# Kernel optimization log

Measured on AMD Instinct MI355X. Metric: run time of the kernel, lower is better.

The kernel has to match this reference:

```python
import jax, jax.numpy as jnp
import numpy as np

N_NODES = 50000
N_EDGES = 800000
D_FEAT = 128
D_HID = 500


def setup_inputs() -> dict:
    key = jax.random.key(0)
    k1, k2, k3, k4 = jax.random.split(key, 4)
    x = jax.random.normal(k1, (N_NODES, D_FEAT), dtype=jnp.float32)
    edge_index = jax.random.randint(k2, (2, N_EDGES), 0, N_NODES, dtype=jnp.int64)
    # Glorot-ish init for weights, zeros for bias (PyG GCNConv default)
    W1 = jax.random.normal(k3, (D_FEAT, D_HID), dtype=jnp.float32) / np.sqrt(D_FEAT)
    b1 = jnp.zeros((D_HID,), dtype=jnp.float32)
    W2 = jax.random.normal(k4, (D_HID, 1), dtype=jnp.float32) / np.sqrt(D_HID)
    b2 = jnp.zeros((1,), dtype=jnp.float32)
    return {"x": x, "edge_index": edge_index, "W1": W1, "b1": b1, "W2": W2, "b2": b2}


def gcn_conv(x, W, b, src, dst, n_nodes):
    """PyG GCNConv: linear transform, add self-loops, symmetric norm, scatter-add, bias."""
    h = x @ W  # [N, out]
    loops = jnp.arange(n_nodes, dtype=src.dtype)
    s = jnp.concatenate([src, loops])  # [E+N]
    d = jnp.concatenate([dst, loops])
    deg = jnp.zeros((n_nodes,), dtype=h.dtype).at[d].add(1.0)
    dinv = jnp.where(deg > 0, jax.lax.rsqrt(deg), 0.0)
    norm = dinv[s] * dinv[d]  # [E+N]
    msg = h[s] * norm[:, None]  # [E+N, out] -- dominant memory traffic
    out = jax.ops.segment_sum(msg, d, num_segments=n_nodes)
    return out + b


def reference(x, edge_index, W1, b1, W2, b2):
    src, dst = edge_index[0], edge_index[1]
    n = x.shape[0]
    h = gcn_conv(x, W1, b1, src, dst, n)
    h = jax.nn.relu(h)
    # F.dropout(training=self.training): identity in eval mode
    out = gcn_conv(h, W2, b2, src, dst, n)
    return out
```

## Files before the change

### kernel.cpp

```cpp
#include <hip/hip_runtime.h>


#define N_NODES 50000
#define N_EDGES 800000
#define D_FEAT  128
#define D_HID   500
#define NTILES  3125
#define BHIST   64
#define EPB     12500
#define SPLIT   5
#define SB      (BHIST * SPLIT)
#define EPSB    (EPB / SPLIT)
#define CONVB   392
#define NGROUP  49
#define GSTRIDE 24576
#define CSRE_SLOTS (NGROUP * GSTRIDE)

typedef __bf16 bf16x8 __attribute__((ext_vector_type(8)));
typedef float  f32x4  __attribute__((ext_vector_type(4)));

static __device__ inline unsigned int f2bf(float f) {
    unsigned int u = __float_as_uint(f);
    return (u + 0x7fffu + ((u >> 16) & 1u)) >> 16;
}
static __device__ inline float bf_lo(unsigned int u) { return __uint_as_float(u << 16); }
static __device__ inline float bf_hi(unsigned int u) { return __uint_as_float(u & 0xffff0000u); }

static __device__ inline void add8(float* acc, uint4 u) {
    acc[0] += bf_lo(u.x);
    acc[1] += bf_hi(u.x);
    acc[2] += bf_lo(u.y);
    acc[3] += bf_hi(u.y);
    acc[4] += bf_lo(u.z);
    acc[5] += bf_hi(u.z);
    acc[6] += bf_lo(u.w);
    acc[7] += bf_hi(u.w);
}

__global__ __launch_bounds__(1024) void k_hist(const int* __restrict__ dst,
                                               const float* __restrict__ W1,
                                               const float* __restrict__ b1,
                                               const float* __restrict__ W2,
                                               unsigned char* __restrict__ coff,
                                               unsigned char* __restrict__ lrank,
                                               unsigned short* __restrict__ b_pk,
                                               float* __restrict__ b1p,
                                               float* __restrict__ w2p) {
    __shared__ unsigned int hist[N_NODES / 4];
    const int b = blockIdx.x, tid = threadIdx.x;
    if (b < BHIST) {
        for (int w = tid; w < N_NODES / 4; w += 1024) hist[w] = 0u;
        __syncthreads();
        const int base = b * EPB;
        for (int i = tid * 4; i < EPB; i += 4096) {
            int4 d4 = *(const int4*)&dst[base + i];
            unsigned int s0 = (unsigned int)(d4.x & 3) * 8u;
            unsigned int s1 = (unsigned int)(d4.y & 3) * 8u;
            unsigned int s2 = (unsigned int)(d4.z & 3) * 8u;
            unsigned int s3 = (unsigned int)(d4.w & 3) * 8u;
            unsigned int r0 = atomicAdd(&hist[d4.x >> 2], 1u << s0);
            unsigned int r1 = atomicAdd(&hist[d4.y >> 2], 1u << s1);
            unsigned int r2 = atomicAdd(&hist[d4.z >> 2], 1u << s2);
            unsigned int r3 = atomicAdd(&hist[d4.w >> 2], 1u << s3);
            uchar4 lr;
            lr.x = (unsigned char)((r0 >> s0) & 0xffu);
            lr.y = (unsigned char)((r1 >> s1) & 0xffu);
            lr.z = (unsigned char)((r2 >> s2) & 0xffu);
            lr.w = (unsigned char)((r3 >> s3) & 0xffu);
            *(uchar4*)&lrank[base + i] = lr;
        }
        __syncthreads();
        unsigned int* crow = (unsigned int*)coff + (size_t)b * (N_NODES / 4);
        for (int w = tid; w < N_NODES / 4; w += 1024) crow[w] = hist[w];
    } else if (b < BHIST + 8) {
        int idx  = (b - BHIST) * 1024 + tid;
        int lane = idx & 63;
        int slot = idx >> 6;
        int t    = slot >> 2;
        int ks   = slot & 3;
        int quad = lane >> 4;
        int n    = t * 16 + (lane & 15);
        unsigned int us[8];
#pragma unroll
        for (int j = 0; j < 8; j++) {
            int k = ks * 32 + quad * 8 + j;
            float v = (n < D_HID) ? W1[(size_t)k * D_HID + n] : 0.f;
            us[j] = f2bf(v);
        }
        uint4 p;
        p.x = us[0] | (us[1] << 16);
        p.y = us[2] | (us[3] << 16);
        p.z = us[4] | (us[5] << 16);
        p.w = us[6] | (us[7] << 16);
        ((uint4*)b_pk)[idx] = p;
    } else {
        if (tid < 512) {
            b1p[tid] = (tid < D_HID) ? b1[tid] : 0.f;
            w2p[tid] = (tid < D_HID) ? W2[tid] : 0.f;
        }
    }
}

__global__ __launch_bounds__(256) void k_scan(unsigned int* __restrict__ coffw,
                                              int* __restrict__ deg,
                                              unsigned int* __restrict__ rstart4) {
    __shared__ unsigned int ps[256];
    const int g = blockIdx.x, tid = threadIdx.x;
    const int idx = g * 256 + tid;
    const bool live = idx < N_NODES / 4;
    unsigned int run0 = 0, run1 = 0, run2 = 0, run3 = 0;
    if (live) {
#pragma unroll 8
        for (int b = 0; b < BHIST; b++) {
            size_t i = (size_t)b * (N_NODES / 4) + idx;
            unsigned int c = coffw[i];
            coffw[i] = run0 | (run1 << 8) | (run2 << 16) | (run3 << 24);
            run0 += c & 0xffu;
            run1 += (c >> 8) & 0xffu;
            run2 += (c >> 16) & 0xffu;
            run3 += (c >> 24) & 0xffu;
        }
        int4 d;
        d.x = (int)run0; d.y = (int)run1; d.z = (int)run2; d.w = (int)run3;
        *(int4*)&deg[idx * 4] = d;
    }
    unsigned int s0 = (run0 + 3u) & ~3u, s1 = (run1 + 3u) & ~3u;
    unsigned int s2 = (run2 + 3u) & ~3u, s3 = (run3 + 3u) & ~3u;
    unsigned int tot = live ? (s0 + s1 + s2 + s3) : 0u;
    ps[tid] = tot;
    __syncthreads();
    for (int off = 1; off < 256; off <<= 1) {
        unsigned int v = (tid >= off) ? ps[tid - off] : 0u;
        __syncthreads();
        ps[tid] += v;
        __syncthreads();
    }
    if (live) {
        unsigned int base = (unsigned int)g * GSTRIDE + (ps[tid] - tot);
        uint4 r;
        r.x = base;
        r.y = base + s0;
        r.z = base + s0 + s1;
        r.w = base + s0 + s1 + s2;
        *(uint4*)&rstart4[idx * 4] = r;
    }
}

__global__ __launch_bounds__(1024) void k_fill(const int* __restrict__ src,
                                               const int* __restrict__ dst,
                                               const unsigned char* __restrict__ coff,
                                               const unsigned char* __restrict__ lrank,
                                               const unsigned int* __restrict__ rstart4,
                                               const int* __restrict__ deg,
                                               const float* __restrict__ x,
                                               unsigned short* __restrict__ csre,
                                               uint2* __restrict__ xd) {
    const int b = blockIdx.x, tid = threadIdx.x;
    if (b < SB) {
        __shared__ unsigned char lcoff[N_NODES];
        const int hb = b / SPLIT;
        const unsigned int* crow =
            (const unsigned int*)coff + (size_t)hb * (N_NODES / 4);
        for (int w = tid; w < N_NODES / 4; w += 1024)
            ((unsigned int*)lcoff)[w] = crow[w];
        __syncthreads();
        const int base = b * EPSB;
        for (int i = tid * 4; i < EPSB; i += 4096) {
            int4 s4 = *(const int4*)&src[base + i];
            int4 d4 = *(const int4*)&dst[base + i];
            uchar4 lr = *(const uchar4*)&lrank[base + i];
            unsigned int t0 = rstart4[d4.x] + (unsigned int)lcoff[d4.x] + lr.x;
            unsigned int t1 = rstart4[d4.y] + (unsigned int)lcoff[d4.y] + lr.y;
            unsigned int t2 = rstart4[d4.z] + (unsigned int)lcoff[d4.z] + lr.z;
            unsigned int t3 = rstart4[d4.w] + (unsigned int)lcoff[d4.w] + lr.w;
            if (t0 < CSRE_SLOTS) csre[t0] = (unsigned short)s4.x;
            if (t1 < CSRE_SLOTS) csre[t1] = (unsigned short)s4.y;
            if (t2 < CSRE_SLOTS) csre[t2] = (unsigned short)s4.z;
            if (t3 < CSRE_SLOTS) csre[t3] = (unsigned short)s4.w;
        }
    } else {
        int gid = (b - SB) * 1024 + tid;
        for (int i = gid; i < N_NODES * D_FEAT / 4; i += CONVB * 1024) {
            float dv = rsqrtf((float)(deg[i >> 5] + 1));
            float4 v = ((const float4*)x)[i];
            uint2 o;
            o.x = f2bf(dv * v.x) | (f2bf(dv * v.y) << 16);
            o.y = f2bf(dv * v.z) | (f2bf(dv * v.w) << 16);
            xd[i] = o;
        }
    }
}

__global__ __launch_bounds__(256, 8) void k_gcn1(const uint4* __restrict__ xd4,
                                                 const unsigned short* __restrict__ csre,
                                                 const unsigned int* __restrict__ rstart4,
                                                 const int* __restrict__ deg,
                                                 const unsigned short* __restrict__ b_pk,
                                                 const float* __restrict__ b1p,
                                                 const float* __restrict__ w2p,
                                                 float* __restrict__ zd) {
    __shared__ unsigned short A[16][136];
    __shared__ float red[4][16];
    const int t = threadIdx.x;
    const int node0 = blockIdx.x * 16;
    const int wv = t >> 6, lane = t & 63;
    const int q = lane >> 4, p = lane & 15;

    {
        const int n = wv * 4 + q;
        const int node = node0 + n;
        int dg = deg[node];
        const unsigned int base = rstart4[node];
        uint4 su = xd4[(size_t)node * 16 + p];
        if (dg > 64) dg = 64;
        float acc[8];
#pragma unroll
        for (int j = 0; j < 8; j++) acc[j] = 0.f;

        int e = 0;
        for (; e + 4 <= dg; e += 4) {
            ushort4 s4 = *(const ushort4*)&csre[base + e];
            uint4 u0 = xd4[(size_t)s4.x * 16 + p];
            uint4 u1 = xd4[(size_t)s4.y * 16 + p];
            uint4 u2 = xd4[(size_t)s4.z * 16 + p];
            uint4 u3 = xd4[(size_t)s4.w * 16 + p];
            add8(acc, u0);
            add8(acc, u1);
            add8(acc, u2);
            add8(acc, u3);
        }
        for (; e < dg; e++) {
            int s = csre[base + e];
            uint4 u = xd4[(size_t)s * 16 + p];
            add8(acc, u);
        }

        const float di = rsqrtf((float)(dg + 1));
        uint4 o;
        o.x = f2bf(di * (acc[0] + bf_lo(su.x))) |
              (f2bf(di * (acc[1] + bf_hi(su.x))) << 16);
        o.y = f2bf(di * (acc[2] + bf_lo(su.y))) |
              (f2bf(di * (acc[3] + bf_hi(su.y))) << 16);
        o.z = f2bf(di * (acc[4] + bf_lo(su.z))) |
              (f2bf(di * (acc[5] + bf_hi(su.z))) << 16);
        o.w = f2bf(di * (acc[6] + bf_lo(su.w))) |
              (f2bf(di * (acc[7] + bf_hi(su.w))) << 16);
        *(uint4*)&A[n][p * 8] = o;
    }
    __syncthreads();

    bf16x8 afr[4];
#pragma unroll
    for (int ks = 0; ks < 4; ks++)
        afr[ks] = *(const bf16x8*)&A[p][ks * 32 + q * 8];

    const bf16x8* __restrict__ bpk = (const bf16x8*)b_pk;
    f32x4 acc[8];
#pragma unroll
    for (int tt = 0; tt < 8; tt++) acc[tt] = (f32x4){0.f, 0.f, 0.f, 0.f};
#pragma unroll
    for (int tt = 0; tt < 8; tt++) {
        const int tile_n = wv * 8 + tt;
#pragma unroll
        for (int ks = 0; ks < 4; ks++) {
            bf16x8 bfr = bpk[(size_t)(tile_n * 4 + ks) * 64 + lane];
            acc[tt] = __builtin_amdgcn_mfma_f32_16x16x32_bf16(afr[ks], bfr, acc[tt], 0, 0, 0);
        }
    }

    float zp[4] = {0.f, 0.f, 0.f, 0.f};
#pragma unroll
    for (int tt = 0; tt < 8; tt++) {
        const int c = (wv * 8 + tt) * 16 + p;
        const float b1v = b1p[c];
        const float w2v = w2p[c];
#pragma unroll
        for (int r = 0; r < 4; r++)
            zp[r] += fmaxf(acc[tt][r] + b1v, 0.f) * w2v;
    }
#pragma unroll
    for (int off = 1; off < 16; off <<= 1) {
#pragma unroll
        for (int r = 0; r < 4; r++) zp[r] += __shfl_xor(zp[r], off);
    }
    if (p == 0) {
#pragma unroll
        for (int r = 0; r < 4; r++) red[wv][q * 4 + r] = zp[r];
    }
    __syncthreads();
    if (t < 16) {
        int node = node0 + t;
        float zz = red[0][t] + red[1][t] + red[2][t] + red[3][t];
        zd[node] = rsqrtf((float)(deg[node] + 1)) * zz;
    }
}

__global__ __launch_bounds__(256) void k_gz(const unsigned short* __restrict__ csre,
                                            const unsigned int* __restrict__ rstart4,
                                            const int* __restrict__ deg,
                                            const float* __restrict__ zd,
                                            const float* __restrict__ b2,
                                            float* __restrict__ out) {
    const int node = blockIdx.x * 16 + (threadIdx.x >> 4);
    const int l = threadIdx.x & 15;
    int dg = deg[node];
    if (dg > 64) dg = 64;
    const unsigned int base = rstart4[node];
    float s = 0.f;
    for (int e = l; e < dg; e += 16) s += zd[csre[base + e]];
#pragma unroll
    for (int off = 1; off < 16; off <<= 1) s += __shfl_xor(s, off);
    if (l == 0) {
        float di = rsqrtf((float)(dg + 1));
        out[node] = di * (s + zd[node]) + b2[0];
    }
}

extern "C" void kernel_launch(void* const* d_in, const int* in_sizes, int n_in,
                              void* d_out, int out_size, void* d_ws, size_t ws_size,
                              hipStream_t stream) {
    const float* x  = (const float*)d_in[0];
    const int*   ei = (const int*)d_in[1];
    const float* W1 = (const float*)d_in[2];
    const float* b1 = (const float*)d_in[3];
    const float* W2 = (const float*)d_in[4];
    const float* b2 = (const float*)d_in[5];
    float* out = (float*)d_out;

    const int* src = ei;
    const int* dst = ei + N_EDGES;

    uint2* xd            = (uint2*)d_ws;
    unsigned short* b_pk = (unsigned short*)(xd + 1600000);
    float* b1p    = (float*)(b_pk + 65536);
    float* w2p    = b1p + 512;
    float* zd     = w2p + 512;
    int* deg      = (int*)(zd + N_NODES);
    unsigned int* rstart4 = (unsigned int*)(deg + N_NODES);
    unsigned char* coff  = (unsigned char*)(rstart4 + N_NODES);
    unsigned char* lrank = coff + (size_t)BHIST * N_NODES;
    unsigned short* csre = (unsigned short*)(lrank + N_EDGES);

    k_hist<<<BHIST + 9, 1024, 0, stream>>>(dst, W1, b1, W2, coff, lrank,
                                           b_pk, b1p, w2p);
    k_scan<<<NGROUP, 256, 0, stream>>>((unsigned int*)coff, deg, rstart4);
    k_fill<<<SB + CONVB, 1024, 0, stream>>>(src, dst, coff, lrank, rstart4,
                                            deg, x, csre, xd);
    k_gcn1<<<NTILES, 256, 0, stream>>>((const uint4*)xd, csre, rstart4, deg,
                                       b_pk, b1p, w2p, zd);
    k_gz  <<<NTILES, 256, 0, stream>>>(csre, rstart4, deg, zd, b2, out);
}
```

Baseline: 153.1 us.

## Fuse hist, scan and fill kernels into one persistent kernel with global flags

The three preprocessing kernels (histogram, scan, CSR fill plus feature scaling) become a single launch of 256 blocks that coordinate through global atomic flags and spin-waits. Blocks finished with earlier stages then help convert features, and the histogram split changes from 64x12500 to 50x16000 edges. This removes two kernel launch boundaries and their idle tails. It relies on all 256 blocks being co-resident, which holds on a 256-CU part, so it risks deadlock on smaller devices. It also adds a memset launch and spin overhead.

```diff
diff --git a/kernel.cpp b/kernel.cpp
--- a/kernel.cpp
+++ b/kernel.cpp
@@ -6,15 +6,17 @@
 #define D_FEAT  128
 #define D_HID   500
 #define NTILES  3125
-#define BHIST   64
-#define EPB     12500
-#define SPLIT   5
-#define SB      (BHIST * SPLIT)
-#define EPSB    (EPB / SPLIT)
-#define CONVB   392
-#define NGROUP  49
+#define BHIST   50
+#define EPB     16000
+#define NSCAN   49
+#define SSPLIT  2
+#define SBLK    (BHIST * SSPLIT)
+#define EPSB    (EPB / SSPLIT)
+#define CONVB   48
+#define NCONV   (SBLK + CONVB + BHIST + NSCAN)
+#define PACK0   (BHIST + NSCAN + SBLK + CONVB)
 #define GSTRIDE 24576
-#define CSRE_SLOTS (NGROUP * GSTRIDE)
+#define CSRE_SLOTS (NSCAN * GSTRIDE)
 
 typedef __bf16 bf16x8 __attribute__((ext_vector_type(8)));
 typedef float  f32x4  __attribute__((ext_vector_type(4)));
@@ -37,19 +39,33 @@
     acc[7] += bf_hi(u.w);
 }
 
-__global__ __launch_bounds__(1024) void k_hist(const int* __restrict__ dst,
-                                               const float* __restrict__ W1,
-                                               const float* __restrict__ b1,
-                                               const float* __restrict__ W2,
-                                               unsigned char* __restrict__ coff,
-                                               unsigned char* __restrict__ lrank,
-                                               unsigned short* __restrict__ b_pk,
-                                               float* __restrict__ b1p,
-                                               float* __restrict__ w2p) {
-    __shared__ unsigned int hist[N_NODES / 4];
+static __device__ inline void spin_until(const int* f, int want) {
+    while (__hip_atomic_load(f, __ATOMIC_ACQUIRE, __HIP_MEMORY_SCOPE_AGENT) < want)
+        __builtin_amdgcn_s_sleep(8);
+}
+
+__global__ __launch_bounds__(1024) void k_build(const int* __restrict__ src,
+                                                const int* __restrict__ dst,
+                                                const float* __restrict__ x,
+                                                const float* __restrict__ W1,
+                                                const float* __restrict__ b1,
+                                                const float* __restrict__ W2,
+                                                unsigned char* __restrict__ coff,
+                                                unsigned char* __restrict__ lrank,
+                                                unsigned int* __restrict__ rstart4,
+                                                int* __restrict__ deg,
+                                                unsigned short* __restrict__ csre,
+                                                uint2* __restrict__ xd,
+                                                unsigned short* __restrict__ b_pk,
+                                                float* __restrict__ b1p,
+                                                float* __restrict__ w2p,
+                                                int* __restrict__ flags) {
+    __shared__ unsigned int sbuf[N_NODES / 4];
     const int b = blockIdx.x, tid = threadIdx.x;
+    int cid = -1;
+
     if (b < BHIST) {
-        for (int w = tid; w < N_NODES / 4; w += 1024) hist[w] = 0u;
+        for (int w = tid; w < N_NODES / 4; w += 1024) sbuf[w] = 0u;
         __syncthreads();
         const int base = b * EPB;
         for (int i = tid * 4; i < EPB; i += 4096) {
@@ -58,10 +74,10 @@
             unsigned int s1 = (unsigned int)(d4.y & 3) * 8u;
             unsigned int s2 = (unsigned int)(d4.z & 3) * 8u;
             unsigned int s3 = (unsigned int)(d4.w & 3) * 8u;
-            unsigned int r0 = atomicAdd(&hist[d4.x >> 2], 1u << s0);
-            unsigned int r1 = atomicAdd(&hist[d4.y >> 2], 1u << s1);
-            unsigned int r2 = atomicAdd(&hist[d4.z >> 2], 1u << s2);
-            unsigned int r3 = atomicAdd(&hist[d4.w >> 2], 1u << s3);
+            unsigned int r0 = atomicAdd(&sbuf[d4.x >> 2], 1u << s0);
+            unsigned int r1 = atomicAdd(&sbuf[d4.y >> 2], 1u << s1);
+            unsigned int r2 = atomicAdd(&sbuf[d4.z >> 2], 1u << s2);
+            unsigned int r3 = atomicAdd(&sbuf[d4.w >> 2], 1u << s3);
             uchar4 lr;
             lr.x = (unsigned char)((r0 >> s0) & 0xffu);
             lr.y = (unsigned char)((r1 >> s1) & 0xffu);
@@ -71,9 +87,96 @@
         }
         __syncthreads();
         unsigned int* crow = (unsigned int*)coff + (size_t)b * (N_NODES / 4);
-        for (int w = tid; w < N_NODES / 4; w += 1024) crow[w] = hist[w];
-    } else if (b < BHIST + 8) {
-        int idx  = (b - BHIST) * 1024 + tid;
+        for (int w = tid; w < N_NODES / 4; w += 1024) crow[w] = sbuf[w];
+        __threadfence();
+        __syncthreads();
+        if (tid == 0)
+            __hip_atomic_fetch_add(&flags[0], 1, __ATOMIC_RELEASE,
+                                   __HIP_MEMORY_SCOPE_AGENT);
+        if (tid == 0) spin_until(&flags[1], NSCAN);
+        __syncthreads();
+        cid = SBLK + CONVB + b;
+    } else if (b < BHIST + NSCAN) {
+        const int g = b - BHIST;
+        if (tid == 0) spin_until(&flags[0], BHIST);
+        __syncthreads();
+        const int w = g * 256 + tid;
+        const bool live = (tid < 256) && (w < N_NODES / 4);
+        unsigned int run0 = 0, run1 = 0, run2 = 0, run3 = 0;
+        if (live) {
+            unsigned int* coffw = (unsigned int*)coff;
+#pragma unroll 10
+            for (int r = 0; r < BHIST; r++) {
+                size_t i = (size_t)r * (N_NODES / 4) + w;
+                unsigned int c = coffw[i];
+                coffw[i] = run0 | (run1 << 8) | (run2 << 16) | (run3 << 24);
+                run0 += c & 0xffu;
+                run1 += (c >> 8) & 0xffu;
+                run2 += (c >> 16) & 0xffu;
+                run3 += (c >> 24) & 0xffu;
+            }
+            int4 d;
+            d.x = (int)run0; d.y = (int)run1; d.z = (int)run2; d.w = (int)run3;
+            *(int4*)&deg[w * 4] = d;
+        }
+        unsigned int s0 = (run0 + 3u) & ~3u, s1 = (run1 + 3u) & ~3u;
+        unsigned int s2 = (run2 + 3u) & ~3u, s3 = (run3 + 3u) & ~3u;
+        unsigned int tot = live ? (s0 + s1 + s2 + s3) : 0u;
+        if (tid < 256) sbuf[tid] = tot;
+        __syncthreads();
+        for (int off = 1; off < 256; off <<= 1) {
+            unsigned int v = 0;
+            if (tid < 256 && tid >= off) v = sbuf[tid - off];
+            __syncthreads();
+            if (tid < 256) sbuf[tid] += v;
+            __syncthreads();
+        }
+        if (live) {
+            unsigned int base = (unsigned int)g * GSTRIDE + (sbuf[tid] - tot);
+            uint4 r;
+            r.x = base;
+            r.y = base + s0;
+            r.z = base + s0 + s1;
+            r.w = base + s0 + s1 + s2;
+            *(uint4*)&rstart4[w * 4] = r;
+        }
+        __threadfence();
+        __syncthreads();
+        if (tid == 0)
+            __hip_atomic_fetch_add(&flags[1], 1, __ATOMIC_RELEASE,
+                                   __HIP_MEMORY_SCOPE_AGENT);
+        cid = SBLK + CONVB + BHIST + g;
+    } else if (b < BHIST + NSCAN + SBLK + CONVB) {
+        if (tid == 0) spin_until(&flags[1], NSCAN);
+        __syncthreads();
+        if (b < BHIST + NSCAN + SBLK) {
+            const int bs = b - BHIST - NSCAN;
+            const int hb = bs >> 1;
+            const unsigned int* crow =
+                (const unsigned int*)coff + (size_t)hb * (N_NODES / 4);
+            for (int w = tid; w < N_NODES / 4; w += 1024) sbuf[w] = crow[w];
+            __syncthreads();
+            const unsigned char* lcoff = (const unsigned char*)sbuf;
+            const int base = hb * EPB + (bs & 1) * EPSB;
+            for (int i = tid * 4; i < EPSB; i += 4096) {
+                int4 s4 = *(const int4*)&src[base + i];
+                int4 d4 = *(const int4*)&dst[base + i];
+                uchar4 lr = *(const uchar4*)&lrank[base + i];
+                unsigned int t0 = rstart4[d4.x] + (unsigned int)lcoff[d4.x] + lr.x;
+                unsigned int t1 = rstart4[d4.y] + (unsigned int)lcoff[d4.y] + lr.y;
+                unsigned int t2 = rstart4[d4.z] + (unsigned int)lcoff[d4.z] + lr.z;
+                unsigned int t3 = rstart4[d4.w] + (unsigned int)lcoff[d4.w] + lr.w;
+                if (t0 < CSRE_SLOTS) csre[t0] = (unsigned short)s4.x;
+                if (t1 < CSRE_SLOTS) csre[t1] = (unsigned short)s4.y;
+                if (t2 < CSRE_SLOTS) csre[t2] = (unsigned short)s4.z;
+                if (t3 < CSRE_SLOTS) csre[t3] = (unsigned short)s4.w;
+            }
+            cid = bs;
+        } else {
+            cid = SBLK + (b - BHIST - NSCAN - SBLK);
+        }
+    } else if (b < PACK0 + 8) {
+        int idx  = (b - PACK0) * 1024 + tid;
         int lane = idx & 63;
         int slot = idx >> 6;
         int t    = slot >> 2;
@@ -93,101 +196,22 @@
         p.z = us[4] | (us[5] << 16);
         p.w = us[6] | (us[7] << 16);
         ((uint4*)b_pk)[idx] = p;
+        return;
     } else {
         if (tid < 512) {
             b1p[tid] = (tid < D_HID) ? b1[tid] : 0.f;
             w2p[tid] = (tid < D_HID) ? W2[tid] : 0.f;
         }
-    }
-}
-
-__global__ __launch_bounds__(256) void k_scan(unsigned int* __restrict__ coffw,
-                                              int* __restrict__ deg,
-                                              unsigned int* __restrict__ rstart4) {
-    __shared__ unsigned int ps[256];
-    const int g = blockIdx.x, tid = threadIdx.x;
-    const int idx = g * 256 + tid;
-    const bool live = idx < N_NODES / 4;
-    unsigned int run0 = 0, run1 = 0, run2 = 0, run3 = 0;
-    if (live) {
-#pragma unroll 8
-        for (int b = 0; b < BHIST; b++) {
-            size_t i = (size_t)b * (N_NODES / 4) + idx;
-            unsigned int c = coffw[i];
-            coffw[i] = run0 | (run1 << 8) | (run2 << 16) | (run3 << 24);
-            run0 += c & 0xffu;
-            run1 += (c >> 8) & 0xffu;
-            run2 += (c >> 16) & 0xffu;
-            run3 += (c >> 24) & 0xffu;
-        }
-        int4 d;
-        d.x = (int)run0; d.y = (int)run1; d.z = (int)run2; d.w = (int)run3;
-        *(int4*)&deg[idx * 4] = d;
-    }
-    unsigned int s0 = (run0 + 3u) & ~3u, s1 = (run1 + 3u) & ~3u;
-    unsigned int s2 = (run2 + 3u) & ~3u, s3 = (run3 + 3u) & ~3u;
-    unsigned int tot = live ? (s0 + s1 + s2 + s3) : 0u;
-    ps[tid] = tot;
-    __syncthreads();
-    for (int off = 1; off < 256; off <<= 1) {
-        unsigned int v = (tid >= off) ? ps[tid - off] : 0u;
-        __syncthreads();
-        ps[tid] += v;
-        __syncthreads();
-    }
-    if (live) {
-        unsigned int base = (unsigned int)g * GSTRIDE + (ps[tid] - tot);
-        uint4 r;
-        r.x = base;
-        r.y = base + s0;
-        r.z = base + s0 + s1;
-        r.w = base + s0 + s1 + s2;
-        *(uint4*)&rstart4[idx * 4] = r;
-    }
-}
-
-__global__ __launch_bounds__(1024) void k_fill(const int* __restrict__ src,
-                                               const int* __restrict__ dst,
-                                               const unsigned char* __restrict__ coff,
-                                               const unsigned char* __restrict__ lrank,
-                                               const unsigned int* __restrict__ rstart4,
-                                               const int* __restrict__ deg,
-                                               const float* __restrict__ x,
-                                               unsigned short* __restrict__ csre,
-                                               uint2* __restrict__ xd) {
-    const int b = blockIdx.x, tid = threadIdx.x;
-    if (b < SB) {
-        __shared__ unsigned char lcoff[N_NODES];
-        const int hb = b / SPLIT;
-        const unsigned int* crow =
-            (const unsigned int*)coff + (size_t)hb * (N_NODES / 4);
-        for (int w = tid; w < N_NODES / 4; w += 1024)
-            ((unsigned int*)lcoff)[w] = crow[w];
-        __syncthreads();
-        const int base = b * EPSB;
-        for (int i = tid * 4; i < EPSB; i += 4096) {
-            int4 s4 = *(const int4*)&src[base + i];
-            int4 d4 = *(const int4*)&dst[base + i];
-            uchar4 lr = *(const uchar4*)&lrank[base + i];
-            unsigned int t0 = rstart4[d4.x] + (unsigned int)lcoff[d4.x] + lr.x;
-            unsigned int t1 = rstart4[d4.y] + (unsigned int)lcoff[d4.y] + lr.y;
-            unsigned int t2 = rstart4[d4.z] + (unsigned int)lcoff[d4.z] + lr.z;
-            unsigned int t3 = rstart4[d4.w] + (unsigned int)lcoff[d4.w] + lr.w;
-            if (t0 < CSRE_SLOTS) csre[t0] = (unsigned short)s4.x;
-            if (t1 < CSRE_SLOTS) csre[t1] = (unsigned short)s4.y;
-            if (t2 < CSRE_SLOTS) csre[t2] = (unsigned short)s4.z;
-            if (t3 < CSRE_SLOTS) csre[t3] = (unsigned short)s4.w;
-        }
-    } else {
-        int gid = (b - SB) * 1024 + tid;
-        for (int i = gid; i < N_NODES * D_FEAT / 4; i += CONVB * 1024) {
-            float dv = rsqrtf((float)(deg[i >> 5] + 1));
-            float4 v = ((const float4*)x)[i];
-            uint2 o;
-            o.x = f2bf(dv * v.x) | (f2bf(dv * v.y) << 16);
-            o.y = f2bf(dv * v.z) | (f2bf(dv * v.w) << 16);
-            xd[i] = o;
-        }
+        return;
+    }
+
+    for (int i = cid * 1024 + tid; i < N_NODES * D_FEAT / 4; i += NCONV * 1024) {
+        float dv = rsqrtf((float)(deg[i >> 5] + 1));
+        float4 v = ((const float4*)x)[i];
+        uint2 o;
+        o.x = f2bf(dv * v.x) | (f2bf(dv * v.y) << 16);
+        o.y = f2bf(dv * v.z) | (f2bf(dv * v.w) << 16);
+        xd[i] = o;
     }
 }
 
@@ -340,12 +364,13 @@
     unsigned char* coff  = (unsigned char*)(rstart4 + N_NODES);
     unsigned char* lrank = coff + (size_t)BHIST * N_NODES;
     unsigned short* csre = (unsigned short*)(lrank + N_EDGES);
-
-    k_hist<<<BHIST + 9, 1024, 0, stream>>>(dst, W1, b1, W2, coff, lrank,
-                                           b_pk, b1p, w2p);
-    k_scan<<<NGROUP, 256, 0, stream>>>((unsigned int*)coff, deg, rstart4);
-    k_fill<<<SB + CONVB, 1024, 0, stream>>>(src, dst, coff, lrank, rstart4,
-                                            deg, x, csre, xd);
+    int* flags    = (int*)(csre + CSRE_SLOTS);
+
+    hipMemsetAsync(flags, 0, 16, stream);
+
+    k_build<<<256, 1024, 0, stream>>>(src, dst, x, W1, b1, W2, coff, lrank,
+                                      rstart4, deg, csre, xd, b_pk, b1p, w2p,
+                                      flags);
     k_gcn1<<<NTILES, 256, 0, stream>>>((const uint4*)xd, csre, rstart4, deg,
                                        b_pk, b1p, w2p, zd);
     k_gz  <<<NTILES, 256, 0, stream>>>(csre, rstart4, deg, zd, b2, out);
```

Result: slower. 298.8 us (+95.1%).

## Move x-scaling conversion into scan kernel with locally recomputed degrees

Applied to the files above, without the earlier changes.

The bf16 conversion of x scaled by rsqrt(degree) moves from the fill kernel into the scan kernel. Extra blocks there recompute per-node degrees on their own by summing the histogram counts for their nodes, so this work runs alongside the scan instead of behind it. The scan now writes exclusive offsets to a separate buffer so the raw counts stay readable. The cost is redundant histogram reads and shared-memory atomics in the conversion blocks, plus an extra 3.2MB offset buffer in the workspace.

```diff
diff --git a/kernel.cpp b/kernel.cpp
--- a/kernel.cpp
+++ b/kernel.cpp
@@ -8,13 +8,14 @@
 #define NTILES  3125
 #define BHIST   64
 #define EPB     12500
-#define SPLIT   5
-#define SB      (BHIST * SPLIT)
-#define EPSB    (EPB / SPLIT)
-#define CONVB   392
-#define NGROUP  49
+#define NSCAN   49
+#define NCONVB  199
+#define NPBW    63
+#define SSPLIT  5
+#define SB      (BHIST * SSPLIT)
+#define EPSB    (EPB / SSPLIT)
 #define GSTRIDE 24576
-#define CSRE_SLOTS (NGROUP * GSTRIDE)
+#define CSRE_SLOTS (NSCAN * GSTRIDE)
 
 typedef __bf16 bf16x8 __attribute__((ext_vector_type(8)));
 typedef float  f32x4  __attribute__((ext_vector_type(4)));
@@ -101,93 +102,110 @@
     }
 }
 
-__global__ __launch_bounds__(256) void k_scan(unsigned int* __restrict__ coffw,
-                                              int* __restrict__ deg,
-                                              unsigned int* __restrict__ rstart4) {
-    __shared__ unsigned int ps[256];
-    const int g = blockIdx.x, tid = threadIdx.x;
-    const int idx = g * 256 + tid;
-    const bool live = idx < N_NODES / 4;
-    unsigned int run0 = 0, run1 = 0, run2 = 0, run3 = 0;
-    if (live) {
+__global__ __launch_bounds__(1024) void k_scan2(const unsigned int* __restrict__ coffw,
+                                                unsigned int* __restrict__ boffw,
+                                                int* __restrict__ deg,
+                                                unsigned int* __restrict__ rstart4,
+                                                const float* __restrict__ x,
+                                                uint2* __restrict__ xd) {
+    const int b = blockIdx.x, tid = threadIdx.x;
+    if (b < NSCAN) {
+        __shared__ unsigned int ps[256];
+        const int w = b * 256 + tid;
+        const bool live = (tid < 256) && (w < N_NODES / 4);
+        unsigned int run0 = 0, run1 = 0, run2 = 0, run3 = 0;
+        if (live) {
 #pragma unroll 8
-        for (int b = 0; b < BHIST; b++) {
-            size_t i = (size_t)b * (N_NODES / 4) + idx;
-            unsigned int c = coffw[i];
-            coffw[i] = run0 | (run1 << 8) | (run2 << 16) | (run3 << 24);
-            run0 += c & 0xffu;
-            run1 += (c >> 8) & 0xffu;
-            run2 += (c >> 16) & 0xffu;
-            run3 += (c >> 24) & 0xffu;
-        }
-        int4 d;
-        d.x = (int)run0; d.y = (int)run1; d.z = (int)run2; d.w = (int)run3;
-        *(int4*)&deg[idx * 4] = d;
-    }
-    unsigned int s0 = (run0 + 3u) & ~3u, s1 = (run1 + 3u) & ~3u;
-    unsigned int s2 = (run2 + 3u) & ~3u, s3 = (run3 + 3u) & ~3u;
-    unsigned int tot = live ? (s0 + s1 + s2 + s3) : 0u;
-    ps[tid] = tot;
-    __syncthreads();
-    for (int off = 1; off < 256; off <<= 1) {
-        unsigned int v = (tid >= off) ? ps[tid - off] : 0u;
-        __syncthreads();
-        ps[tid] += v;
-        __syncthreads();
-    }
-    if (live) {
-        unsigned int base = (unsigned int)g * GSTRIDE + (ps[tid] - tot);
-        uint4 r;
-        r.x = base;
-        r.y = base + s0;
-        r.z = base + s0 + s1;
-        r.w = base + s0 + s1 + s2;
-        *(uint4*)&rstart4[idx * 4] = r;
+            for (int r = 0; r < BHIST; r++) {
+                size_t i = (size_t)r * (N_NODES / 4) + w;
+                unsigned int c = coffw[i];
+                boffw[i] = run0 | (run1 << 8) | (run2 << 16) | (run3 << 24);
+                run0 += c & 0xffu;
+                run1 += (c >> 8) & 0xffu;
+                run2 += (c >> 16) & 0xffu;
+                run3 += (c >> 24) & 0xffu;
+            }
+            int4 d;
+            d.x = (int)run0; d.y = (int)run1; d.z = (int)run2; d.w = (int)run3;
+            *(int4*)&deg[w * 4] = d;
+        }
+        unsigned int s0 = (run0 + 3u) & ~3u, s1 = (run1 + 3u) & ~3u;
+        unsigned int s2 = (run2 + 3u) & ~3u, s3 = (run3 + 3u) & ~3u;
+        unsigned int tot = live ? (s0 + s1 + s2 + s3) : 0u;
+        if (tid < 256) ps[tid] = tot;
+        __syncthreads();
+        for (int off = 1; off < 256; off <<= 1) {
+            unsigned int v = 0;
+            if (tid < 256 && tid >= off) v = ps[tid - off];
+            __syncthreads();
+            if (tid < 256) ps[tid] += v;
+            __syncthreads();
+        }
+        if (live) {
+            unsigned int base = (unsigned int)b * GSTRIDE + (ps[tid] - tot);
+            uint4 r;
+            r.x = base;
+            r.y = base + s0;
+            r.z = base + s0 + s1;
+            r.w = base + s0 + s1 + s2;
+            *(uint4*)&rstart4[w * 4] = r;
+        }
+    } else {
+        __shared__ unsigned int ldw[NPBW];
+        const int cb = b - NSCAN;
+        if (tid < NPBW) ldw[tid] = 0u;
+        __syncthreads();
+        for (int k = tid; k < BHIST * NPBW; k += 1024) {
+            int r  = k / NPBW;
+            int wl = k - r * NPBW;
+            int w  = cb * NPBW + wl;
+            if (w < N_NODES / 4)
+                atomicAdd(&ldw[wl], coffw[(size_t)r * (N_NODES / 4) + w]);
+        }
+        __syncthreads();
+        for (int j = tid; j < 252 * 32; j += 1024) {
+            int i = cb * 8064 + j;
+            if (i < N_NODES * D_FEAT / 4) {
+                int nl = j >> 5;
+                unsigned int dgb = (ldw[nl >> 2] >> ((nl & 3) * 8)) & 0xffu;
+                float dv = rsqrtf((float)(dgb + 1u));
+                float4 v = ((const float4*)x)[i];
+                uint2 o;
+                o.x = f2bf(dv * v.x) | (f2bf(dv * v.y) << 16);
+                o.y = f2bf(dv * v.z) | (f2bf(dv * v.w) << 16);
+                xd[i] = o;
+            }
+        }
     }
 }
 
 __global__ __launch_bounds__(1024) void k_fill(const int* __restrict__ src,
                                                const int* __restrict__ dst,
-                                               const unsigned char* __restrict__ coff,
+                                               const unsigned char* __restrict__ boff,
                                                const unsigned char* __restrict__ lrank,
                                                const unsigned int* __restrict__ rstart4,
-                                               const int* __restrict__ deg,
-                                               const float* __restrict__ x,
-                                               unsigned short* __restrict__ csre,
-                                               uint2* __restrict__ xd) {
+                                               unsigned short* __restrict__ csre) {
+    __shared__ unsigned int sbuf[N_NODES / 4];
     const int b = blockIdx.x, tid = threadIdx.x;
-    if (b < SB) {
-        __shared__ unsigned char lcoff[N_NODES];
-        const int hb = b / SPLIT;
-        const unsigned int* crow =
-            (const unsigned int*)coff + (size_t)hb * (N_NODES / 4);
-        for (int w = tid; w < N_NODES / 4; w += 1024)
-            ((unsigned int*)lcoff)[w] = crow[w];
-        __syncthreads();
-        const int base = b * EPSB;
-        for (int i = tid * 4; i < EPSB; i += 4096) {
-            int4 s4 = *(const int4*)&src[base + i];
-            int4 d4 = *(const int4*)&dst[base + i];
-            uchar4 lr = *(const uchar4*)&lrank[base + i];
-            unsigned int t0 = rstart4[d4.x] + (unsigned int)lcoff[d4.x] + lr.x;
-            unsigned int t1 = rstart4[d4.y] + (unsigned int)lcoff[d4.y] + lr.y;
-            unsigned int t2 = rstart4[d4.z] + (unsigned int)lcoff[d4.z] + lr.z;
-            unsigned int t3 = rstart4[d4.w] + (unsigned int)lcoff[d4.w] + lr.w;
-            if (t0 < CSRE_SLOTS) csre[t0] = (unsigned short)s4.x;
-            if (t1 < CSRE_SLOTS) csre[t1] = (unsigned short)s4.y;
-            if (t2 < CSRE_SLOTS) csre[t2] = (unsigned short)s4.z;
-            if (t3 < CSRE_SLOTS) csre[t3] = (unsigned short)s4.w;
-        }
-    } else {
-        int gid = (b - SB) * 1024 + tid;
-        for (int i = gid; i < N_NODES * D_FEAT / 4; i += CONVB * 1024) {
-            float dv = rsqrtf((float)(deg[i >> 5] + 1));
-            float4 v = ((const float4*)x)[i];
-            uint2 o;
-            o.x = f2bf(dv * v.x) | (f2bf(dv * v.y) << 16);
-            o.y = f2bf(dv * v.z) | (f2bf(dv * v.w) << 16);
-            xd[i] = o;
-        }
+    const int hb = b / SSPLIT;
+    const unsigned int* brow =
+        (const unsigned int*)boff + (size_t)hb * (N_NODES / 4);
+    for (int w = tid; w < N_NODES / 4; w += 1024) sbuf[w] = brow[w];
+    __syncthreads();
+    const unsigned char* lcoff = (const unsigned char*)sbuf;
+    const int base = b * EPSB;
+    for (int i = tid * 4; i < EPSB; i += 4096) {
+        int4 s4 = *(const int4*)&src[base + i];
+        int4 d4 = *(const int4*)&dst[base + i];
+        uchar4 lr = *(const uchar4*)&lrank[base + i];
+        unsigned int t0 = rstart4[d4.x] + (unsigned int)lcoff[d4.x] + lr.x;
+        unsigned int t1 = rstart4[d4.y] + (unsigned int)lcoff[d4.y] + lr.y;
+        unsigned int t2 = rstart4[d4.z] + (unsigned int)lcoff[d4.z] + lr.z;
+        unsigned int t3 = rstart4[d4.w] + (unsigned int)lcoff[d4.w] + lr.w;
+        if (t0 < CSRE_SLOTS) csre[t0] = (unsigned short)s4.x;
+        if (t1 < CSRE_SLOTS) csre[t1] = (unsigned short)s4.y;
+        if (t2 < CSRE_SLOTS) csre[t2] = (unsigned short)s4.z;
+        if (t3 < CSRE_SLOTS) csre[t3] = (unsigned short)s4.w;
     }
 }
 
@@ -338,14 +356,16 @@
     int* deg      = (int*)(zd + N_NODES);
     unsigned int* rstart4 = (unsigned int*)(deg + N_NODES);
     unsigned char* coff  = (unsigned char*)(rstart4 + N_NODES);
-    unsigned char* lrank = coff + (size_t)BHIST * N_NODES;
+    unsigned char* boff  = coff + (size_t)BHIST * N_NODES;
+    unsigned char* lrank = boff + (size_t)BHIST * N_NODES;
     unsigned short* csre = (unsigned short*)(lrank + N_EDGES);
 
     k_hist<<<BHIST + 9, 1024, 0, stream>>>(dst, W1, b1, W2, coff, lrank,
                                            b_pk, b1p, w2p);
-    k_scan<<<NGROUP, 256, 0, stream>>>((unsigned int*)coff, deg, rstart4);
-    k_fill<<<SB + CONVB, 1024, 0, stream>>>(src, dst, coff, lrank, rstart4,
-                                            deg, x, csre, xd);
+    k_scan2<<<NSCAN + NCONVB, 1024, 0, stream>>>((unsigned int*)coff,
+                                                 (unsigned int*)boff, deg,
+                                                 rstart4, x, xd);
+    k_fill<<<SB, 1024, 0, stream>>>(src, dst, boff, lrank, rstart4, csre);
     k_gcn1<<<NTILES, 256, 0, stream>>>((const uint4*)xd, csre, rstart4, deg,
                                        b_pk, b1p, w2p, zd);
     k_gz  <<<NTILES, 256, 0, stream>>>(csre, rstart4, deg, zd, b2, out);
```

New measurement: 153.9 us. No clear change (+0.5%).
